# Kernel optimization log

Measured on AMD Instinct MI355X. Metric: run time of the kernel, lower is better.

Reference implementation:

```python
import jax, jax.numpy as jnp
import numpy as np

TEMP = 40.0
POOL = 7          # pooling_resolution
EPS = 1e-5


def setup_inputs() -> dict:
    key = jax.random.key(0)
    ks = jax.random.split(key, 16)
    B, C, H, W = 64, 512, 28, 28
    K = 7                      # kernel_size
    Cb = C // 4                # bottleneck channels
    P2 = POOL * POOL
    inp = {}
    inp["x"] = jax.random.normal(ks[0], (B, C, H, W), dtype=jnp.float32)
    # BatchNorm2d (eval mode: running stats + affine)
    inp["bn_gamma"] = 1.0 + 0.1 * jax.random.normal(ks[1], (C,), dtype=jnp.float32)
    inp["bn_beta"] = 0.1 * jax.random.normal(ks[2], (C,), dtype=jnp.float32)
    inp["bn_mean"] = 0.1 * jax.random.normal(ks[3], (C,), dtype=jnp.float32)
    inp["bn_var"] = jax.random.uniform(ks[4], (C,), minval=0.5, maxval=1.5, dtype=jnp.float32)
    # 1x1 conv weights (no bias)
    inp["Wq"] = jax.random.normal(ks[5], (C, C), dtype=jnp.float32) / np.sqrt(C)
    inp["Wk"] = jax.random.normal(ks[6], (C, C), dtype=jnp.float32) / np.sqrt(C)
    # kernel_layer: Linear(P^2 -> K^2, bias=False); torch weight shape (out,in)
    inp["Wkern"] = jax.random.normal(ks[7], (K * K, P2), dtype=jnp.float32) / np.sqrt(P2)
    # fusion_conv0: 1x1 conv C -> Cb, with bias
    inp["Wf0"] = jax.random.normal(ks[8], (Cb, C), dtype=jnp.float32) / np.sqrt(C)
    inp["bf0"] = 0.1 * jax.random.normal(ks[9], (Cb,), dtype=jnp.float32)
    # LayerNorm([Cb, K, K]) affine
    inp["ln_w"] = 1.0 + 0.1 * jax.random.normal(ks[10], (Cb, K, K), dtype=jnp.float32)
    inp["ln_b"] = 0.1 * jax.random.normal(ks[11], (Cb, K, K), dtype=jnp.float32)
    # fusion_conv1: 1x1 conv Cb -> C, with bias
    inp["Wf1"] = jax.random.normal(ks[12], (C, Cb), dtype=jnp.float32) / np.sqrt(Cb)
    inp["bf1"] = 0.1 * jax.random.normal(ks[13], (C,), dtype=jnp.float32)
    return inp


def reference(x, bn_gamma, bn_beta, bn_mean, bn_var, Wq, Wk, Wkern,
              Wf0, bf0, ln_w, ln_b, Wf1, bf1):
    B, C, H, W = x.shape
    K = int(round(Wkern.shape[0] ** 0.5))

    # AdaptiveAvgPool2d to (POOL, POOL); H, W divisible by POOL
    pooled = x.reshape(B, C, POOL, H // POOL, POOL, W // POOL).mean(axis=(3, 5))
    # BatchNorm2d (eval mode)
    pooled = (pooled - bn_mean[:, None, None]) * (
        bn_gamma[:, None, None] / jnp.sqrt(bn_var[:, None, None] + EPS)
    ) + bn_beta[:, None, None]

    pf = pooled.reshape(B, C, POOL * POOL)            # b c p
    Q = jnp.einsum('oc,bcp->bop', Wq, pf)             # b c p
    Kt = jnp.einsum('oc,bcp->bpo', Wk, pf)            # b p c
    attn = jax.nn.softmax(jnp.einsum('bcp,bpd->bcd', Q, Kt) / TEMP, axis=2)  # b c c

    kw = jnp.einsum('kp,bcp->bck', Wkern, pf)         # b c k^2
    kw = jnp.einsum('bcd,bdk->bck', attn, kw)         # b c k^2
    kw = kw.reshape(B, C, K, K)

    # fusion_conv0 (1x1) + LayerNorm([Cb,K,K]) + tanh + fusion_conv1 (1x1)
    kw = jnp.einsum('oc,bckl->bokl', Wf0, kw) + bf0[:, None, None]
    mu = kw.mean(axis=(1, 2, 3), keepdims=True)
    var = kw.var(axis=(1, 2, 3), keepdims=True)
    kw = (kw - mu) / jnp.sqrt(var + EPS) * ln_w + ln_b
    kw = jnp.tanh(kw)
    kw = jnp.einsum('oc,bckl->bokl', Wf1, kw) + bf1[:, None, None]  # b C K K

    # dynamic depthwise conv: one kernel per (b, c); groups = B*C
    weights = kw.reshape(B * C, 1, K, K)
    out = jax.lax.conv_general_dilated(
        x.reshape(1, B * C, H, W), weights,
        window_strides=(1, 1), padding=[(K // 2, K // 2)] * 2,
        feature_group_count=B * C,
        dimension_numbers=('NCHW', 'OIHW', 'NCHW'))
    return out.reshape(B, C, H, W)
```

## Files before the change

### kernel.cpp

```cpp
#include <hip/hip_runtime.h>
#include <math.h>

#define BB   64
#define CC   512
#define P2   49
#define CB   128
#define NB   3136
#define TEMPI (1.0f/40.0f)

typedef __attribute__((ext_vector_type(4))) short    bf16x4;
typedef __attribute__((ext_vector_type(4))) float    f32x4;
typedef unsigned short u16;

__device__ inline u16 f2bf(float f) {
    union { float f; unsigned u; } x{f};
    unsigned r = (x.u + 0x7FFFu + ((x.u >> 16) & 1u)) >> 16;
    return (u16)r;
}

__device__ inline f32x4 mfma16x16(bf16x4 a, bf16x4 b, f32x4 c) {
#if __has_builtin(__builtin_amdgcn_mfma_f32_16x16x16bf16_1k)
    return __builtin_amdgcn_mfma_f32_16x16x16bf16_1k(a, b, c, 0, 0, 0);
#elif __has_builtin(__builtin_amdgcn_mfma_f32_16x16x16_bf16)
    return __builtin_amdgcn_mfma_f32_16x16x16_bf16(a, b, c, 0, 0, 0);
#else
    f32x4 d;
    asm("v_mfma_f32_16x16x16_bf16 %0, %1, %2, %3"
        : "=v"(d) : "v"(a), "v"(b), "v"(c));
    return d;
#endif
}

__global__ __launch_bounds__(256) void repack_all_k(
    const float* __restrict__ Wq, const float* __restrict__ Wk,
    const float* __restrict__ Wf0, const float* __restrict__ Wf1,
    const float* __restrict__ Wkern,
    u16* __restrict__ WqF, u16* __restrict__ WkF,
    u16* __restrict__ Wf0F, u16* __restrict__ Wf1F,
    u16* __restrict__ WkernF)
{
    int u = blockIdx.x * 256 + threadIdx.x;
    if (u >= 163840) {
        int uu = u - 163840;
        int l = uu & 63, rest = uu >> 6;
        int ct = rest & 3, t = rest >> 2;
        int o  = t * 16 + (l & 15);
        int c0 = ct * 16 + ((l >> 4) << 2);
        ushort4 v;
        v.x = (o < 49 && c0 + 0 < 49) ? f2bf(Wkern[o * 49 + c0 + 0]) : 0;
        v.y = (o < 49 && c0 + 1 < 49) ? f2bf(Wkern[o * 49 + c0 + 1]) : 0;
        v.z = (o < 49 && c0 + 2 < 49) ? f2bf(Wkern[o * 49 + c0 + 2]) : 0;
        v.w = (o < 49 && c0 + 3 < 49) ? f2bf(Wkern[o * 49 + c0 + 3]) : 0;
        ((ushort4*)WkernF)[uu] = v;
        return;
    }
    const float* W; u16* dst; int K, uu;
    if (u < 65536)       { W = Wq;  dst = WqF;  K = 512; uu = u; }
    else if (u < 131072) { W = Wk;  dst = WkF;  K = 512; uu = u - 65536; }
    else if (u < 147456) { W = Wf0; dst = Wf0F; K = 512; uu = u - 131072; }
    else                 { W = Wf1; dst = Wf1F; K = 128; uu = u - 147456; }
    int l = uu & 63, rest = uu >> 6;
    int KT = K >> 4;
    int ct = rest % KT, t = rest / KT;
    int o  = t * 16 + (l & 15);
    int c0 = ct * 16 + ((l >> 4) << 2);
    float4 v = *(const float4*)(W + (size_t)o * K + c0);
    ushort4 w;
    w.x = f2bf(v.x); w.y = f2bf(v.y); w.z = f2bf(v.z); w.w = f2bf(v.w);
    ((ushort4*)dst)[uu] = w;
}

__global__ __launch_bounds__(256) void prep_k(
    const float* __restrict__ x, const float* __restrict__ g,
    const float* __restrict__ be, const float* __restrict__ mu,
    const float* __restrict__ var, const u16* __restrict__ WkernF,
    u16* __restrict__ pfF, u16* __restrict__ VF)
{
    __shared__ float pf[32][50];
    int tid = threadIdx.x;
    int bg  = blockIdx.x;
    int b = bg >> 4, grp = bg & 15;
    int cbase = grp * 32;

    for (int i = tid; i < 32 * 49; i += 256) {
        int cl = i / 49, p = i - cl * 49;
        int c = cbase + cl;
        const float* basep = x + ((size_t)(b * 512 + c)) * 784
                             + (p / 7) * 4 * 28 + (p % 7) * 4;
        float s = 0.f;
#pragma unroll
        for (int r = 0; r < 4; ++r) {
            float4 v = *(const float4*)(basep + r * 28);
            s += v.x + v.y + v.z + v.w;
        }
        s *= (1.f / 16.f);
        float sc = g[c] * rsqrtf(var[c] + 1e-5f);
        pf[cl][p] = (s - mu[c]) * sc + be[c];
    }
    __syncthreads();

    for (int u = tid; u < 512; u += 256) {
        int l = u & 63, q = (u >> 6) & 3, ctl = u >> 8;
        int p   = q * 16 + (l & 15);
        int c0l = ctl * 16 + ((l >> 4) << 2);
        ushort4 o;
        if (p < 49) {
            o.x = f2bf(pf[c0l + 0][p]); o.y = f2bf(pf[c0l + 1][p]);
            o.z = f2bf(pf[c0l + 2][p]); o.w = f2bf(pf[c0l + 3][p]);
        } else { o.x = o.y = o.z = o.w = 0; }
        ((ushort4*)pfF)[((size_t)(b * 32 + grp * 2 + ctl) * 4 + q) * 64 + l] = o;
    }

    int lane = tid & 63, w = tid >> 6;
    const bf16x4* WkF4 = (const bf16x4*)WkernF;
#pragma unroll
    for (int i = 0; i < 2; ++i) {
        int dt  = w * 2 + i;
        int ct2 = dt & 1, tk = dt >> 1;
        int cc  = ct2 * 16 + (lane & 15);
        f32x4 acc = (f32x4)0.f;
#pragma unroll
        for (int ptp = 0; ptp < 4; ++ptp) {
            bf16x4 af;
#pragma unroll
            for (int j = 0; j < 4; ++j) {
                int p = ptp * 16 + ((lane >> 4) << 2) + j;
                af[j] = (short)((p < 49) ? f2bf(pf[cc][p]) : 0);
            }
            bf16x4 bw = WkF4[(tk * 4 + ptp) * 64 + lane];
            acc = mfma16x16(af, bw, acc);
        }
        ushort4 o;
        o.x = f2bf(acc[0]); o.y = f2bf(acc[1]);
        o.z = f2bf(acc[2]); o.w = f2bf(acc[3]);
        ((ushort4*)VF)[((size_t)(b * 32 + grp * 2 + ct2) * 4 + tk) * 64 + lane] = o;
    }
}

__global__ __launch_bounds__(256) void gemm_qk_k(
    const u16* __restrict__ pfF, const u16* __restrict__ WqF,
    const u16* __restrict__ WkF, u16* __restrict__ QF, u16* __restrict__ KF)
{
    const u16* WF   = blockIdx.z ? WkF : WqF;
    u16*       dstF = blockIdx.z ? KF : QF;
    int tid  = threadIdx.x;
    int lane = tid & 63;
    int w    = tid >> 6;
    int b    = blockIdx.y;
    int t    = blockIdx.x * 4 + w;

    const bf16x4* Ab = (const bf16x4*)pfF + (size_t)b * 8192 + lane;
    const bf16x4* Bw = (const bf16x4*)WF + (size_t)t * 2048 + lane;

    f32x4 acc[4];
#pragma unroll
    for (int q = 0; q < 4; ++q) acc[q] = (f32x4)0.f;

#pragma unroll
    for (int ct = 0; ct < 32; ++ct) {
        bf16x4 wv = Bw[ct * 64];
        bf16x4 a0 = Ab[(ct * 4 + 0) * 64];
        bf16x4 a1 = Ab[(ct * 4 + 1) * 64];
        bf16x4 a2 = Ab[(ct * 4 + 2) * 64];
        bf16x4 a3 = Ab[(ct * 4 + 3) * 64];
        acc[0] = mfma16x16(a0, wv, acc[0]);
        acc[1] = mfma16x16(a1, wv, acc[1]);
        acc[2] = mfma16x16(a2, wv, acc[2]);
        acc[3] = mfma16x16(a3, wv, acc[3]);
    }

#pragma unroll
    for (int q = 0; q < 4; ++q) {
        ushort4 u;
        u.x = f2bf(acc[q][0]); u.y = f2bf(acc[q][1]);
        u.z = f2bf(acc[q][2]); u.w = f2bf(acc[q][3]);
        ((ushort4*)dstF)[(((size_t)b * 32 + t) * 4 + q) * 64 + lane] = u;
    }
}

__global__ __launch_bounds__(512) void attn_mfma_k(
    const u16* __restrict__ QF, const u16* __restrict__ KF,
    const u16* __restrict__ VF, u16* __restrict__ OtF)
{
    __shared__ f32x4 po[4][4][64];
    __shared__ float pl[4][64];
    int tid  = threadIdx.x;
    int lane = tid & 63;
    int w    = tid >> 6;
    int wq   = w & 3, half = w >> 2;
    int b    = blockIdx.y;
    int ct   = blockIdx.x * 4 + wq;

    const bf16x4* QFp = (const bf16x4*)QF + (size_t)b * 8192 + ct * 256 + lane;
    const bf16x4* KFp = (const bf16x4*)KF + (size_t)b * 8192 + lane;
    const bf16x4* VFp = (const bf16x4*)VF + (size_t)b * 8192 + lane;

    bf16x4 qf[4];
#pragma unroll
    for (int q = 0; q < 4; ++q) qf[q] = QFp[q * 64];

    f32x4 o[4];
#pragma unroll
    for (int pt = 0; pt < 4; ++pt) o[pt] = (f32x4)0.f;
    float lsum = 0.f;

    int t0 = half * 16;
    bf16x4 kf[4], vf[4], kn[4], vn[4];
#pragma unroll
    for (int q = 0; q < 4; ++q) {
        kf[q] = KFp[(t0 * 4 + q) * 64];
        vf[q] = VFp[(t0 * 4 + q) * 64];
    }

    for (int tt = 0; tt < 16; ++tt) {
        if (tt < 15) {
            const bf16x4* kp = KFp + (t0 + tt + 1) * 256;
            const bf16x4* vp = VFp + (t0 + tt + 1) * 256;
#pragma unroll
            for (int q = 0; q < 4; ++q) { kn[q] = kp[q * 64]; vn[q] = vp[q * 64]; }
        }
        f32x4 s = (f32x4)0.f;
#pragma unroll
        for (int q = 0; q < 4; ++q) s = mfma16x16(kf[q], qf[q], s);

        bf16x4 pa;
#pragma unroll
        for (int r = 0; r < 4; ++r) {
            float pe = __expf(s[r] * TEMPI);
            lsum += pe;
            pa[r] = (short)f2bf(pe);
        }
#pragma unroll
        for (int pt = 0; pt < 4; ++pt) o[pt] = mfma16x16(pa, vf[pt], o[pt]);

#pragma unroll
        for (int q = 0; q < 4; ++q) { kf[q] = kn[q]; vf[q] = vn[q]; }
    }

    if (half == 1) {
#pragma unroll
        for (int pt = 0; pt < 4; ++pt) po[wq][pt][lane] = o[pt];
        pl[wq][lane] = lsum;
    }
    __syncthreads();
    if (half == 1) return;
#pragma unroll
    for (int pt = 0; pt < 4; ++pt) {
        f32x4 t = po[wq][pt][lane];
        o[pt][0] += t[0]; o[pt][1] += t[1]; o[pt][2] += t[2]; o[pt][3] += t[3];
    }
    lsum += pl[wq][lane];

    lsum += __shfl_xor(lsum, 16);
    lsum += __shfl_xor(lsum, 32);
    float linv = 1.f / lsum;

    int g4 = (lane >> 4) << 2;
    float rl0 = __shfl(linv, g4 + 0);
    float rl1 = __shfl(linv, g4 + 1);
    float rl2 = __shfl(linv, g4 + 2);
    float rl3 = __shfl(linv, g4 + 3);

#pragma unroll
    for (int pt = 0; pt < 4; ++pt) {
        ushort4 u;
        u.x = f2bf(o[pt][0] * rl0);
        u.y = f2bf(o[pt][1] * rl1);
        u.z = f2bf(o[pt][2] * rl2);
        u.w = f2bf(o[pt][3] * rl3);
        ((ushort4*)OtF)[(((size_t)b * 32 + ct) * 4 + pt) * 64 + lane] = u;
    }
}

__global__ __launch_bounds__(512) void f0ln_k(
    const u16* __restrict__ OtF, const u16* __restrict__ Wf0F,
    const float* __restrict__ bf0, const float* __restrict__ lnw,
    const float* __restrict__ lnb, u16* __restrict__ GF)
{
    __shared__ float F0[128][50];
    __shared__ float rs[8], rq[8];
    __shared__ float smu, srstd;
    int tid  = threadIdx.x;
    int lane = tid & 63, w = tid >> 6;
    int b = blockIdx.x;

    const bf16x4* Ab = (const bf16x4*)OtF + (size_t)b * 8192 + lane;
    const bf16x4* Bw = (const bf16x4*)Wf0F + (size_t)w * 2048 + lane;

    f32x4 acc[4];
#pragma unroll
    for (int q = 0; q < 4; ++q) acc[q] = (f32x4)0.f;
#pragma unroll
    for (int ct = 0; ct < 32; ++ct) {
        bf16x4 wv = Bw[ct * 64];
        bf16x4 a0 = Ab[(ct * 4 + 0) * 64];
        bf16x4 a1 = Ab[(ct * 4 + 1) * 64];
        bf16x4 a2 = Ab[(ct * 4 + 2) * 64];
        bf16x4 a3 = Ab[(ct * 4 + 3) * 64];
        acc[0] = mfma16x16(a0, wv, acc[0]);
        acc[1] = mfma16x16(a1, wv, acc[1]);
        acc[2] = mfma16x16(a2, wv, acc[2]);
        acc[3] = mfma16x16(a3, wv, acc[3]);
    }

    int c = w * 16 + (lane & 15);
    float bb = bf0[c];
    int g4 = (lane >> 4) << 2;
#pragma unroll
    for (int q = 0; q < 4; ++q)
#pragma unroll
        for (int r = 0; r < 4; ++r) {
            int p = q * 16 + g4 + r;
            if (p < 49) F0[c][p] = acc[q][r] + bb;
        }
    __syncthreads();

    float s = 0.f, sq = 0.f;
    for (int e = tid; e < CB * 49; e += 512) {
        int o = e / 49, k = e - o * 49;
        float v = F0[o][k];
        s += v; sq += v * v;
    }
#pragma unroll
    for (int off = 32; off > 0; off >>= 1) {
        s  += __shfl_xor(s, off);
        sq += __shfl_xor(sq, off);
    }
    if ((tid & 63) == 0) { rs[w] = s; rq[w] = sq; }
    __syncthreads();
    if (tid == 0) {
        float S = 0.f, Q = 0.f;
#pragma unroll
        for (int i = 0; i < 8; ++i) { S += rs[i]; Q += rq[i]; }
        float mu = S / 6272.f;
        float v  = Q / 6272.f - mu * mu;
        smu = mu; srstd = rsqrtf(v + 1e-5f);
    }
    __syncthreads();
    float mu = smu, rstd = srstd;

    for (int u = tid; u < 2048; u += 512) {
        int l = u & 63, q = (u >> 6) & 3, ct = u >> 8;
        int c0 = ct * 16 + ((l >> 4) << 2);
        int k  = q * 16 + (l & 15);
        ushort4 o;
        if (k < 49) {
            o.x = f2bf(tanhf((F0[c0+0][k] - mu) * rstd * lnw[(c0+0)*49+k] + lnb[(c0+0)*49+k]));
            o.y = f2bf(tanhf((F0[c0+1][k] - mu) * rstd * lnw[(c0+1)*49+k] + lnb[(c0+1)*49+k]));
            o.z = f2bf(tanhf((F0[c0+2][k] - mu) * rstd * lnw[(c0+2)*49+k] + lnb[(c0+2)*49+k]));
            o.w = f2bf(tanhf((F0[c0+3][k] - mu) * rstd * lnw[(c0+3)*49+k] + lnb[(c0+3)*49+k]));
        } else { o.x = o.y = o.z = o.w = 0; }
        ((ushort4*)GF)[(((size_t)b * 8 + ct) * 4 + q) * 64 + l] = o;
    }
}

template <int KT>
__global__ __launch_bounds__(256) void fusion_frag_k(
    const u16* __restrict__ AF, const u16* __restrict__ WF,
    float* __restrict__ Cout, const float* __restrict__ bias)
{
    int tid  = threadIdx.x;
    int lane = tid & 63;
    int w    = tid >> 6;
    int b    = blockIdx.y;
    int t    = blockIdx.x * 4 + w;

    const bf16x4* Ab = (const bf16x4*)AF + (size_t)b * (KT * 256) + lane;
    const bf16x4* Bw = (const bf16x4*)WF + (size_t)t * (KT * 64) + lane;

    f32x4 acc[4];
#pragma unroll
    for (int q = 0; q < 4; ++q) acc[q] = (f32x4)0.f;

#pragma unroll
    for (int ct = 0; ct < KT; ++ct) {
        bf16x4 wv = Bw[ct * 64];
        bf16x4 a0 = Ab[(ct * 4 + 0) * 64];
        bf16x4 a1 = Ab[(ct * 4 + 1) * 64];
        bf16x4 a2 = Ab[(ct * 4 + 2) * 64];
        bf16x4 a3 = Ab[(ct * 4 + 3) * 64];
        acc[0] = mfma16x16(a0, wv, acc[0]);
        acc[1] = mfma16x16(a1, wv, acc[1]);
        acc[2] = mfma16x16(a2, wv, acc[2]);
        acc[3] = mfma16x16(a3, wv, acc[3]);
    }

    int c = t * 16 + (lane & 15);
    float bb = bias[c];
    float* op = Cout + (size_t)c * NB + b * 49;
    int g4 = (lane >> 4) << 2;
#pragma unroll
    for (int q = 0; q < 4; ++q) {
#pragma unroll
        for (int r = 0; r < 4; ++r) {
            int p = q * 16 + g4 + r;
            if (p < 49) op[p] = acc[q][r] + bb;
        }
    }
}

#define PLS 1256
__global__ __launch_bounds__(256) void dwconv_k(
    const float* __restrict__ x, const float* __restrict__ KernT,
    float* __restrict__ out)
{
    __shared__ float xs[4 * PLS];
    int tid  = threadIdx.x;
    int lane = tid & 63;
    int wid  = tid >> 6;
    int P    = blockIdx.x * 4 + wid;
    int b = P >> 9, c = P & 511;
    float* pl = &xs[wid * PLS];

    float4* plf = (float4*)pl;
#pragma unroll
    for (int r = 0; r < 5; ++r) {
        int l = lane + 64 * r;
        if (l < PLS / 4) plf[l] = float4{0.f, 0.f, 0.f, 0.f};
    }

    float wvl = 0.f;
    if (lane < 49) wvl = KernT[(size_t)c * NB + b * 49 + lane];
    int wvi = __float_as_int(wvl);
    float w[49];
#pragma unroll
    for (int i = 0; i < 49; ++i)
        w[i] = __int_as_float(__builtin_amdgcn_readlane(wvi, i));

    const float* src = x + (size_t)P * 784;
#pragma unroll
    for (int r = 0; r < 4; ++r) {
        int q = lane + 64 * r;
        if (q < 196) {
            int y = q / 7, xq = 4 * (q % 7);
            int R = y + 3;
            *(float4*)&pl[R * 36 + (((R >> 2) & 7) << 2) + xq + 4] =
                *(const float4*)(src + y * 28 + xq);
        }
    }

    if (lane >= 49) return;
    int ty = lane / 7, gx = lane - ty * 7;
    int y0 = 4 * ty, x0 = 4 * gx;
    float acc[4][4] = {};

#pragma unroll
    for (int yy = 0; yy < 10; ++yy) {
        int R = y0 + yy;
        const float* rp = &pl[R * 36 + (((R >> 2) & 7) << 2) + x0];
        float4 fa = *(const float4*)(rp);
        float4 fb = *(const float4*)(rp + 4);
        float4 fc = *(const float4*)(rp + 8);
        float f[12] = {fa.x, fa.y, fa.z, fa.w, fb.x, fb.y, fb.z, fb.w,
                       fc.x, fc.y, fc.z, fc.w};
#pragma unroll
        for (int j = 0; j < 4; ++j) {
            int dy = yy - j;
            if (dy < 0 || dy > 6) continue;
#pragma unroll
            for (int dx = 0; dx < 7; ++dx) {
                float wv = w[dy * 7 + dx];
                acc[j][0] = fmaf(wv, f[dx + 1], acc[j][0]);
                acc[j][1] = fmaf(wv, f[dx + 2], acc[j][1]);
                acc[j][2] = fmaf(wv, f[dx + 3], acc[j][2]);
                acc[j][3] = fmaf(wv, f[dx + 4], acc[j][3]);
            }
        }
    }

    float* op = out + (size_t)P * 784;
#pragma unroll
    for (int j = 0; j < 4; ++j) {
        float4 o4 = {acc[j][0], acc[j][1], acc[j][2], acc[j][3]};
        *(float4*)(op + (y0 + j) * 28 + x0) = o4;
    }
}

extern "C" void kernel_launch(void* const* d_in, const int* in_sizes, int n_in,
                              void* d_out, int out_size, void* d_ws, size_t ws_size,
                              hipStream_t stream)
{
    const float* x     = (const float*)d_in[0];
    const float* bng   = (const float*)d_in[1];
    const float* bnb   = (const float*)d_in[2];
    const float* bnm   = (const float*)d_in[3];
    const float* bnv   = (const float*)d_in[4];
    const float* Wq    = (const float*)d_in[5];
    const float* Wk    = (const float*)d_in[6];
    const float* Wkern = (const float*)d_in[7];
    const float* Wf0   = (const float*)d_in[8];
    const float* bf0   = (const float*)d_in[9];
    const float* lnw   = (const float*)d_in[10];
    const float* lnb   = (const float*)d_in[11];
    const float* Wf1   = (const float*)d_in[12];
    const float* bf1   = (const float*)d_in[13];
    float* out = (float*)d_out;
    float* ws  = (float*)d_ws;

    u16* pfF    = (u16*)(ws + 0);
    u16* VF     = (u16*)(ws + 1048576);
    u16* WqF    = (u16*)(ws + 2097152);
    u16* WkF    = (u16*)(ws + 2228224);
    u16* Wf0F   = (u16*)(ws + 2359296);
    u16* Wf1F   = (u16*)(ws + 2392064);
    u16* WkernF = (u16*)(ws + 2424832);
    u16* QF     = (u16*)(ws + 2426880);
    u16* KF     = (u16*)(ws + 3475456);
    u16* OtF    = (u16*)(ws + 4524032);
    u16* GF     = (u16*)(ws + 5572608);
    float* KernT = ws + 2426880;

    repack_all_k<<<644, 256, 0, stream>>>(Wq, Wk, Wf0, Wf1, Wkern,
                                          WqF, WkF, Wf0F, Wf1F, WkernF);
    prep_k<<<1024, 256, 0, stream>>>(x, bng, bnb, bnm, bnv, WkernF, pfF, VF);
    gemm_qk_k<<<dim3(8, 64, 2), 256, 0, stream>>>(pfF, WqF, WkF, QF, KF);
    attn_mfma_k<<<dim3(8, 64), 512, 0, stream>>>(QF, KF, VF, OtF);
    f0ln_k<<<64, 512, 0, stream>>>(OtF, Wf0F, bf0, lnw, lnb, GF);
    fusion_frag_k<8><<<dim3(8, 64), 256, 0, stream>>>(GF, Wf1F, KernT, bf1);
    dwconv_k<<<8192, 256, 0, stream>>>(x, KernT, out);
}
```

Baseline: 160.8 us.

## Fuse QK GEMM, attention, fusion conv0+LN and conv1 into one per-batch kernel

```diff
diff --git a/kernel.cpp b/kernel.cpp
--- a/kernel.cpp
+++ b/kernel.cpp
@@ -137,264 +137,236 @@
     }
 }
 
-__global__ __launch_bounds__(256) void gemm_qk_k(
+__global__ __launch_bounds__(512) void mega_k(
     const u16* __restrict__ pfF, const u16* __restrict__ WqF,
-    const u16* __restrict__ WkF, u16* __restrict__ QF, u16* __restrict__ KF)
-{
-    const u16* WF   = blockIdx.z ? WkF : WqF;
-    u16*       dstF = blockIdx.z ? KF : QF;
-    int tid  = threadIdx.x;
-    int lane = tid & 63;
-    int w    = tid >> 6;
-    int b    = blockIdx.y;
-    int t    = blockIdx.x * 4 + w;
-
-    const bf16x4* Ab = (const bf16x4*)pfF + (size_t)b * 8192 + lane;
-    const bf16x4* Bw = (const bf16x4*)WF + (size_t)t * 2048 + lane;
-
-    f32x4 acc[4];
-#pragma unroll
-    for (int q = 0; q < 4; ++q) acc[q] = (f32x4)0.f;
-
-#pragma unroll
-    for (int ct = 0; ct < 32; ++ct) {
-        bf16x4 wv = Bw[ct * 64];
-        bf16x4 a0 = Ab[(ct * 4 + 0) * 64];
-        bf16x4 a1 = Ab[(ct * 4 + 1) * 64];
-        bf16x4 a2 = Ab[(ct * 4 + 2) * 64];
-        bf16x4 a3 = Ab[(ct * 4 + 3) * 64];
-        acc[0] = mfma16x16(a0, wv, acc[0]);
-        acc[1] = mfma16x16(a1, wv, acc[1]);
-        acc[2] = mfma16x16(a2, wv, acc[2]);
-        acc[3] = mfma16x16(a3, wv, acc[3]);
-    }
-
-#pragma unroll
-    for (int q = 0; q < 4; ++q) {
-        ushort4 u;
-        u.x = f2bf(acc[q][0]); u.y = f2bf(acc[q][1]);
-        u.z = f2bf(acc[q][2]); u.w = f2bf(acc[q][3]);
-        ((ushort4*)dstF)[(((size_t)b * 32 + t) * 4 + q) * 64 + lane] = u;
-    }
-}
-
-__global__ __launch_bounds__(512) void attn_mfma_k(
-    const u16* __restrict__ QF, const u16* __restrict__ KF,
-    const u16* __restrict__ VF, u16* __restrict__ OtF)
-{
-    __shared__ f32x4 po[4][4][64];
-    __shared__ float pl[4][64];
-    int tid  = threadIdx.x;
-    int lane = tid & 63;
-    int w    = tid >> 6;
-    int wq   = w & 3, half = w >> 2;
-    int b    = blockIdx.y;
-    int ct   = blockIdx.x * 4 + wq;
-
-    const bf16x4* QFp = (const bf16x4*)QF + (size_t)b * 8192 + ct * 256 + lane;
-    const bf16x4* KFp = (const bf16x4*)KF + (size_t)b * 8192 + lane;
-    const bf16x4* VFp = (const bf16x4*)VF + (size_t)b * 8192 + lane;
-
-    bf16x4 qf[4];
-#pragma unroll
-    for (int q = 0; q < 4; ++q) qf[q] = QFp[q * 64];
-
-    f32x4 o[4];
-#pragma unroll
-    for (int pt = 0; pt < 4; ++pt) o[pt] = (f32x4)0.f;
-    float lsum = 0.f;
-
-    int t0 = half * 16;
-    bf16x4 kf[4], vf[4], kn[4], vn[4];
-#pragma unroll
-    for (int q = 0; q < 4; ++q) {
-        kf[q] = KFp[(t0 * 4 + q) * 64];
-        vf[q] = VFp[(t0 * 4 + q) * 64];
-    }
-
-    for (int tt = 0; tt < 16; ++tt) {
-        if (tt < 15) {
-            const bf16x4* kp = KFp + (t0 + tt + 1) * 256;
-            const bf16x4* vp = VFp + (t0 + tt + 1) * 256;
-#pragma unroll
-            for (int q = 0; q < 4; ++q) { kn[q] = kp[q * 64]; vn[q] = vp[q * 64]; }
-        }
-        f32x4 s = (f32x4)0.f;
-#pragma unroll
-        for (int q = 0; q < 4; ++q) s = mfma16x16(kf[q], qf[q], s);
-
-        bf16x4 pa;
-#pragma unroll
-        for (int r = 0; r < 4; ++r) {
-            float pe = __expf(s[r] * TEMPI);
-            lsum += pe;
-            pa[r] = (short)f2bf(pe);
-        }
-#pragma unroll
-        for (int pt = 0; pt < 4; ++pt) o[pt] = mfma16x16(pa, vf[pt], o[pt]);
-
-#pragma unroll
-        for (int q = 0; q < 4; ++q) { kf[q] = kn[q]; vf[q] = vn[q]; }
-    }
-
-    if (half == 1) {
-#pragma unroll
-        for (int pt = 0; pt < 4; ++pt) po[wq][pt][lane] = o[pt];
-        pl[wq][lane] = lsum;
-    }
-    __syncthreads();
-    if (half == 1) return;
-#pragma unroll
-    for (int pt = 0; pt < 4; ++pt) {
-        f32x4 t = po[wq][pt][lane];
-        o[pt][0] += t[0]; o[pt][1] += t[1]; o[pt][2] += t[2]; o[pt][3] += t[3];
-    }
-    lsum += pl[wq][lane];
-
-    lsum += __shfl_xor(lsum, 16);
-    lsum += __shfl_xor(lsum, 32);
-    float linv = 1.f / lsum;
-
-    int g4 = (lane >> 4) << 2;
-    float rl0 = __shfl(linv, g4 + 0);
-    float rl1 = __shfl(linv, g4 + 1);
-    float rl2 = __shfl(linv, g4 + 2);
-    float rl3 = __shfl(linv, g4 + 3);
-
-#pragma unroll
-    for (int pt = 0; pt < 4; ++pt) {
-        ushort4 u;
-        u.x = f2bf(o[pt][0] * rl0);
-        u.y = f2bf(o[pt][1] * rl1);
-        u.z = f2bf(o[pt][2] * rl2);
-        u.w = f2bf(o[pt][3] * rl3);
-        ((ushort4*)OtF)[(((size_t)b * 32 + ct) * 4 + pt) * 64 + lane] = u;
-    }
-}
-
-__global__ __launch_bounds__(512) void f0ln_k(
-    const u16* __restrict__ OtF, const u16* __restrict__ Wf0F,
-    const float* __restrict__ bf0, const float* __restrict__ lnw,
-    const float* __restrict__ lnb, u16* __restrict__ GF)
+    const u16* __restrict__ WkF, u16* __restrict__ QF, u16* __restrict__ KF,
+    const u16* __restrict__ VF, u16* __restrict__ OtF,
+    const u16* __restrict__ Wf0F, const float* __restrict__ bf0,
+    const float* __restrict__ lnw, const float* __restrict__ lnb,
+    const u16* __restrict__ Wf1F, const float* __restrict__ bf1,
+    float* __restrict__ KernT)
 {
     __shared__ float F0[128][50];
+    __shared__ ushort4 GfLds[32][64];
     __shared__ float rs[8], rq[8];
     __shared__ float smu, srstd;
+
     int tid  = threadIdx.x;
     int lane = tid & 63, w = tid >> 6;
-    int b = blockIdx.x;
-
-    const bf16x4* Ab = (const bf16x4*)OtF + (size_t)b * 8192 + lane;
-    const bf16x4* Bw = (const bf16x4*)Wf0F + (size_t)w * 2048 + lane;
-
-    f32x4 acc[4];
-#pragma unroll
-    for (int q = 0; q < 4; ++q) acc[q] = (f32x4)0.f;
-#pragma unroll
-    for (int ct = 0; ct < 32; ++ct) {
-        bf16x4 wv = Bw[ct * 64];
-        bf16x4 a0 = Ab[(ct * 4 + 0) * 64];
-        bf16x4 a1 = Ab[(ct * 4 + 1) * 64];
-        bf16x4 a2 = Ab[(ct * 4 + 2) * 64];
-        bf16x4 a3 = Ab[(ct * 4 + 3) * 64];
-        acc[0] = mfma16x16(a0, wv, acc[0]);
-        acc[1] = mfma16x16(a1, wv, acc[1]);
-        acc[2] = mfma16x16(a2, wv, acc[2]);
-        acc[3] = mfma16x16(a3, wv, acc[3]);
-    }
-
-    int c = w * 16 + (lane & 15);
-    float bb = bf0[c];
-    int g4 = (lane >> 4) << 2;
-#pragma unroll
-    for (int q = 0; q < 4; ++q)
-#pragma unroll
-        for (int r = 0; r < 4; ++r) {
-            int p = q * 16 + g4 + r;
-            if (p < 49) F0[c][p] = acc[q][r] + bb;
-        }
+    int b    = blockIdx.x;
+
+    {
+        const bf16x4* Ab = (const bf16x4*)pfF + (size_t)b * 8192 + lane;
+#pragma unroll
+        for (int z = 0; z < 2; ++z) {
+            const u16* WF = z ? WkF : WqF;
+            u16* dstF = z ? KF : QF;
+#pragma unroll
+            for (int i = 0; i < 4; ++i) {
+                int t = w + 8 * i;
+                const bf16x4* Bw = (const bf16x4*)WF + (size_t)t * 2048 + lane;
+                f32x4 acc[4];
+#pragma unroll
+                for (int q = 0; q < 4; ++q) acc[q] = (f32x4)0.f;
+#pragma unroll
+                for (int ct = 0; ct < 32; ++ct) {
+                    bf16x4 wv = Bw[ct * 64];
+                    bf16x4 a0 = Ab[(ct * 4 + 0) * 64];
+                    bf16x4 a1 = Ab[(ct * 4 + 1) * 64];
+                    bf16x4 a2 = Ab[(ct * 4 + 2) * 64];
+                    bf16x4 a3 = Ab[(ct * 4 + 3) * 64];
+                    acc[0] = mfma16x16(a0, wv, acc[0]);
+                    acc[1] = mfma16x16(a1, wv, acc[1]);
+                    acc[2] = mfma16x16(a2, wv, acc[2]);
+                    acc[3] = mfma16x16(a3, wv, acc[3]);
+                }
+#pragma unroll
+                for (int q = 0; q < 4; ++q) {
+                    ushort4 u;
+                    u.x = f2bf(acc[q][0]); u.y = f2bf(acc[q][1]);
+                    u.z = f2bf(acc[q][2]); u.w = f2bf(acc[q][3]);
+                    ((ushort4*)dstF)[(((size_t)b * 32 + t) * 4 + q) * 64 + lane] = u;
+                }
+            }
+        }
+    }
     __syncthreads();
 
-    float s = 0.f, sq = 0.f;
-    for (int e = tid; e < CB * 49; e += 512) {
-        int o = e / 49, k = e - o * 49;
-        float v = F0[o][k];
-        s += v; sq += v * v;
-    }
-#pragma unroll
-    for (int off = 32; off > 0; off >>= 1) {
-        s  += __shfl_xor(s, off);
-        sq += __shfl_xor(sq, off);
-    }
-    if ((tid & 63) == 0) { rs[w] = s; rq[w] = sq; }
+    {
+        const bf16x4* KFp = (const bf16x4*)KF + (size_t)b * 8192 + lane;
+        const bf16x4* VFp = (const bf16x4*)VF + (size_t)b * 8192 + lane;
+#pragma unroll
+        for (int i = 0; i < 4; ++i) {
+            int ct = w + 8 * i;
+            const bf16x4* QFp = (const bf16x4*)QF + (size_t)b * 8192 + ct * 256 + lane;
+
+            bf16x4 qf[4];
+#pragma unroll
+            for (int q = 0; q < 4; ++q) qf[q] = QFp[q * 64];
+
+            f32x4 o[4];
+#pragma unroll
+            for (int pt = 0; pt < 4; ++pt) o[pt] = (f32x4)0.f;
+            float lsum = 0.f;
+
+            bf16x4 kf[4], vf[4], kn[4], vn[4];
+#pragma unroll
+            for (int q = 0; q < 4; ++q) { kf[q] = KFp[q * 64]; vf[q] = VFp[q * 64]; }
+
+            for (int t = 0; t < 32; ++t) {
+                if (t < 31) {
+                    const bf16x4* kp = KFp + (t + 1) * 256;
+                    const bf16x4* vp = VFp + (t + 1) * 256;
+#pragma unroll
+                    for (int q = 0; q < 4; ++q) { kn[q] = kp[q * 64]; vn[q] = vp[q * 64]; }
+                }
+                f32x4 s = (f32x4)0.f;
+#pragma unroll
+                for (int q = 0; q < 4; ++q) s = mfma16x16(kf[q], qf[q], s);
+
+                bf16x4 pa;
+#pragma unroll
+                for (int r = 0; r < 4; ++r) {
+                    float pe = __expf(s[r] * TEMPI);
+                    lsum += pe;
+                    pa[r] = (short)f2bf(pe);
+                }
+#pragma unroll
+                for (int pt = 0; pt < 4; ++pt) o[pt] = mfma16x16(pa, vf[pt], o[pt]);
+
+#pragma unroll
+                for (int q = 0; q < 4; ++q) { kf[q] = kn[q]; vf[q] = vn[q]; }
+            }
+
+            lsum += __shfl_xor(lsum, 16);
+            lsum += __shfl_xor(lsum, 32);
+            float linv = 1.f / lsum;
+
+            int g4 = (lane >> 4) << 2;
+            float rl0 = __shfl(linv, g4 + 0);
+            float rl1 = __shfl(linv, g4 + 1);
+            float rl2 = __shfl(linv, g4 + 2);
+            float rl3 = __shfl(linv, g4 + 3);
+
+#pragma unroll
+            for (int pt = 0; pt < 4; ++pt) {
+                ushort4 u;
+                u.x = f2bf(o[pt][0] * rl0);
+                u.y = f2bf(o[pt][1] * rl1);
+                u.z = f2bf(o[pt][2] * rl2);
+                u.w = f2bf(o[pt][3] * rl3);
+                ((ushort4*)OtF)[(((size_t)b * 32 + ct) * 4 + pt) * 64 + lane] = u;
+            }
+        }
+    }
     __syncthreads();
-    if (tid == 0) {
-        float S = 0.f, Q = 0.f;
-#pragma unroll
-        for (int i = 0; i < 8; ++i) { S += rs[i]; Q += rq[i]; }
-        float mu = S / 6272.f;
-        float v  = Q / 6272.f - mu * mu;
-        smu = mu; srstd = rsqrtf(v + 1e-5f);
+
+    {
+        const bf16x4* Ab = (const bf16x4*)OtF + (size_t)b * 8192 + lane;
+        const bf16x4* Bw = (const bf16x4*)Wf0F + (size_t)w * 2048 + lane;
+
+        f32x4 acc[4];
+#pragma unroll
+        for (int q = 0; q < 4; ++q) acc[q] = (f32x4)0.f;
+#pragma unroll
+        for (int ct = 0; ct < 32; ++ct) {
+            bf16x4 wv = Bw[ct * 64];
+            bf16x4 a0 = Ab[(ct * 4 + 0) * 64];
+            bf16x4 a1 = Ab[(ct * 4 + 1) * 64];
+            bf16x4 a2 = Ab[(ct * 4 + 2) * 64];
+            bf16x4 a3 = Ab[(ct * 4 + 3) * 64];
+            acc[0] = mfma16x16(a0, wv, acc[0]);
+            acc[1] = mfma16x16(a1, wv, acc[1]);
+            acc[2] = mfma16x16(a2, wv, acc[2]);
+            acc[3] = mfma16x16(a3, wv, acc[3]);
+        }
+
+        int c = w * 16 + (lane & 15);
+        float bb = bf0[c];
+        int g4 = (lane >> 4) << 2;
+#pragma unroll
+        for (int q = 0; q < 4; ++q)
+#pragma unroll
+            for (int r = 0; r < 4; ++r) {
+                int p = q * 16 + g4 + r;
+                if (p < 49) F0[c][p] = acc[q][r] + bb;
+            }
+        __syncthreads();
+
+        float s = 0.f, sq = 0.f;
+        for (int e = tid; e < CB * 49; e += 512) {
+            int o = e / 49, k = e - o * 49;
+            float v = F0[o][k];
+            s += v; sq += v * v;
+        }
+#pragma unroll
+        for (int off = 32; off > 0; off >>= 1) {
+            s  += __shfl_xor(s, off);
+            sq += __shfl_xor(sq, off);
+        }
+        if ((tid & 63) == 0) { rs[w] = s; rq[w] = sq; }
+        __syncthreads();
+        if (tid == 0) {
+            float S = 0.f, Q = 0.f;
+#pragma unroll
+            for (int i = 0; i < 8; ++i) { S += rs[i]; Q += rq[i]; }
+            float mu = S / 6272.f;
+            float v  = Q / 6272.f - mu * mu;
+            smu = mu; srstd = rsqrtf(v + 1e-5f);
+        }
+        __syncthreads();
+        float mu = smu, rstd = srstd;
+
+        for (int u = tid; u < 2048; u += 512) {
+            int l = u & 63, q = (u >> 6) & 3, ct = u >> 8;
+            int c0 = ct * 16 + ((l >> 4) << 2);
+            int k  = q * 16 + (l & 15);
+            ushort4 o;
+            if (k < 49) {
+                o.x = f2bf(tanhf((F0[c0+0][k] - mu) * rstd * lnw[(c0+0)*49+k] + lnb[(c0+0)*49+k]));
+                o.y = f2bf(tanhf((F0[c0+1][k] - mu) * rstd * lnw[(c0+1)*49+k] + lnb[(c0+1)*49+k]));
+                o.z = f2bf(tanhf((F0[c0+2][k] - mu) * rstd * lnw[(c0+2)*49+k] + lnb[(c0+2)*49+k]));
+                o.w = f2bf(tanhf((F0[c0+3][k] - mu) * rstd * lnw[(c0+3)*49+k] + lnb[(c0+3)*49+k]));
+            } else { o.x = o.y = o.z = o.w = 0; }
+            GfLds[ct * 4 + q][l] = o;
+        }
     }
     __syncthreads();
-    float mu = smu, rstd = srstd;
-
-    for (int u = tid; u < 2048; u += 512) {
-        int l = u & 63, q = (u >> 6) & 3, ct = u >> 8;
-        int c0 = ct * 16 + ((l >> 4) << 2);
-        int k  = q * 16 + (l & 15);
-        ushort4 o;
-        if (k < 49) {
-            o.x = f2bf(tanhf((F0[c0+0][k] - mu) * rstd * lnw[(c0+0)*49+k] + lnb[(c0+0)*49+k]));
-            o.y = f2bf(tanhf((F0[c0+1][k] - mu) * rstd * lnw[(c0+1)*49+k] + lnb[(c0+1)*49+k]));
-            o.z = f2bf(tanhf((F0[c0+2][k] - mu) * rstd * lnw[(c0+2)*49+k] + lnb[(c0+2)*49+k]));
-            o.w = f2bf(tanhf((F0[c0+3][k] - mu) * rstd * lnw[(c0+3)*49+k] + lnb[(c0+3)*49+k]));
-        } else { o.x = o.y = o.z = o.w = 0; }
-        ((ushort4*)GF)[(((size_t)b * 8 + ct) * 4 + q) * 64 + l] = o;
-    }
-}
-
-template <int KT>
-__global__ __launch_bounds__(256) void fusion_frag_k(
-    const u16* __restrict__ AF, const u16* __restrict__ WF,
-    float* __restrict__ Cout, const float* __restrict__ bias)
-{
-    int tid  = threadIdx.x;
-    int lane = tid & 63;
-    int w    = tid >> 6;
-    int b    = blockIdx.y;
-    int t    = blockIdx.x * 4 + w;
-
-    const bf16x4* Ab = (const bf16x4*)AF + (size_t)b * (KT * 256) + lane;
-    const bf16x4* Bw = (const bf16x4*)WF + (size_t)t * (KT * 64) + lane;
-
-    f32x4 acc[4];
-#pragma unroll
-    for (int q = 0; q < 4; ++q) acc[q] = (f32x4)0.f;
-
-#pragma unroll
-    for (int ct = 0; ct < KT; ++ct) {
-        bf16x4 wv = Bw[ct * 64];
-        bf16x4 a0 = Ab[(ct * 4 + 0) * 64];
-        bf16x4 a1 = Ab[(ct * 4 + 1) * 64];
-        bf16x4 a2 = Ab[(ct * 4 + 2) * 64];
-        bf16x4 a3 = Ab[(ct * 4 + 3) * 64];
-        acc[0] = mfma16x16(a0, wv, acc[0]);
-        acc[1] = mfma16x16(a1, wv, acc[1]);
-        acc[2] = mfma16x16(a2, wv, acc[2]);
-        acc[3] = mfma16x16(a3, wv, acc[3]);
-    }
-
-    int c = t * 16 + (lane & 15);
-    float bb = bias[c];
-    float* op = Cout + (size_t)c * NB + b * 49;
-    int g4 = (lane >> 4) << 2;
-#pragma unroll
-    for (int q = 0; q < 4; ++q) {
-#pragma unroll
-        for (int r = 0; r < 4; ++r) {
-            int p = q * 16 + g4 + r;
-            if (p < 49) op[p] = acc[q][r] + bb;
+
+    {
+#pragma unroll
+        for (int i = 0; i < 4; ++i) {
+            int t = w + 8 * i;
+            const bf16x4* Bw = (const bf16x4*)Wf1F + (size_t)t * 512 + lane;
+
+            f32x4 acc[4];
+#pragma unroll
+            for (int q = 0; q < 4; ++q) acc[q] = (f32x4)0.f;
+#pragma unroll
+            for (int ct = 0; ct < 8; ++ct) {
+                bf16x4 wv = Bw[ct * 64];
+                bf16x4 a0 = *(bf16x4*)&GfLds[ct * 4 + 0][lane];
+                bf16x4 a1 = *(bf16x4*)&GfLds[ct * 4 + 1][lane];
+                bf16x4 a2 = *(bf16x4*)&GfLds[ct * 4 + 2][lane];
+                bf16x4 a3 = *(bf16x4*)&GfLds[ct * 4 + 3][lane];
+                acc[0] = mfma16x16(a0, wv, acc[0]);
+                acc[1] = mfma16x16(a1, wv, acc[1]);
+                acc[2] = mfma16x16(a2, wv, acc[2]);
+                acc[3] = mfma16x16(a3, wv, acc[3]);
+            }
+
+            int c = t * 16 + (lane & 15);
+            float bb = bf1[c];
+            float* op = KernT + (size_t)c * NB + b * 49;
+            int g4 = (lane >> 4) << 2;
+#pragma unroll
+            for (int q = 0; q < 4; ++q) {
+#pragma unroll
+                for (int r = 0; r < 4; ++r) {
+                    int p = q * 16 + g4 + r;
+                    if (p < 49) op[p] = acc[q][r] + bb;
+                }
+            }
         }
     }
 }
@@ -507,15 +479,12 @@
     u16* QF     = (u16*)(ws + 2426880);
     u16* KF     = (u16*)(ws + 3475456);
     u16* OtF    = (u16*)(ws + 4524032);
-    u16* GF     = (u16*)(ws + 5572608);
-    float* KernT = ws + 2426880;
+    float* KernT = ws + 5572608;
 
     repack_all_k<<<644, 256, 0, stream>>>(Wq, Wk, Wf0, Wf1, Wkern,
                                           WqF, WkF, Wf0F, Wf1F, WkernF);
     prep_k<<<1024, 256, 0, stream>>>(x, bng, bnb, bnm, bnv, WkernF, pfF, VF);
-    gemm_qk_k<<<dim3(8, 64, 2), 256, 0, stream>>>(pfF, WqF, WkF, QF, KF);
-    attn_mfma_k<<<dim3(8, 64), 512, 0, stream>>>(QF, KF, VF, OtF);
-    f0ln_k<<<64, 512, 0, stream>>>(OtF, Wf0F, bf0, lnw, lnb, GF);
-    fusion_frag_k<8><<<dim3(8, 64), 256, 0, stream>>>(GF, Wf1F, KernT, bf1);
+    mega_k<<<64, 512, 0, stream>>>(pfF, WqF, WkF, QF, KF, VF, OtF,
+                                   Wf0F, bf0, lnw, lnb, Wf1F, bf1, KernT);
     dwconv_k<<<8192, 256, 0, stream>>>(x, KernT, out);
 }
```

Result: slower. 296.6 us (+84.4%).
